# Optimization experiments

Hardware: AMD Instinct MI355X
Metric: run time of the kernel (lower is better)

The kernel has to match this reference:

```python
import jax, jax.numpy as jnp
import numpy as np

N_NODES = 100000


def _add_self_loops(edge_index, n):
    loop = jnp.arange(n, dtype=edge_index.dtype)
    src = jnp.concatenate([edge_index[0], loop])
    dst = jnp.concatenate([edge_index[1], loop])
    return src, dst


def _gcn_conv(x, W, b, src, dst, n):
    # PyG GCNConv: add_self_loops + symmetric normalization + linear + scatter-add
    deg = jax.ops.segment_sum(jnp.ones_like(dst, dtype=x.dtype), dst, num_segments=n)
    dinv = jnp.where(deg > 0, jax.lax.rsqrt(deg), 0.0)
    h = x @ W  # [N, F_out]
    norm = dinv[src] * dinv[dst]            # [E]
    msg = h[src] * norm[:, None]            # gather + scale, [E, F_out]
    out = jax.ops.segment_sum(msg, dst, num_segments=n)
    return out + b


def setup_inputs() -> dict:
    key = jax.random.key(0)
    k1, k2, k3, k4 = jax.random.split(key, 4)
    d = 128
    E = 1600000
    x = jax.random.normal(k1, (N_NODES, d), dtype=jnp.float32)
    edge_index = jax.random.randint(k2, (2, E), 0, N_NODES, dtype=jnp.int64)
    # Glorot-ish scaling for the linear weights
    s = 1.0 / np.sqrt(d)
    W1 = jax.random.normal(k3, (d, d), dtype=jnp.float32) * s
    W2 = jax.random.normal(k4, (d, d), dtype=jnp.float32) * s
    b1 = jnp.zeros((d,), dtype=jnp.float32)
    b2 = jnp.zeros((d,), dtype=jnp.float32)
    return {"x": x, "edge_index": edge_index, "W1": W1, "b1": b1, "W2": W2, "b2": b2}


def reference(x, edge_index, W1, b1, W2, b2):
    n = x.shape[0]
    src, dst = _add_self_loops(edge_index, n)
    h = jax.nn.relu(_gcn_conv(x, W1, b1, src, dst, n))
    out = _gcn_conv(h, W2, b2, src, dst, n)
    # original does x.view(1600) (= N * out_channels for its 40x40 toy size);
    # generalized: flatten to [N * out_channels]
    return out.reshape(-1)
```

## Files before the change

kernel.cpp:

```cpp
#include <hip/hip_runtime.h>

static inline int idiv_up(int a, int b) { return (a + b - 1) / b; }

typedef __attribute__((ext_vector_type(8))) short bf16x8;
typedef __attribute__((ext_vector_type(4))) float f32x4;

#define NBSHIFT 10
#define BCAP    20480
#define EPB     4096

__device__ __forceinline__ float bf16u_to_f32(unsigned short u) {
    return __uint_as_float(((unsigned int)u) << 16);
}

__device__ __forceinline__ unsigned short f32_to_bf16u(float x) {
    unsigned int b = __float_as_uint(x);
    b += 0x7FFFu + ((b >> 16) & 1u);
    return (unsigned short)(b >> 16);
}

__global__ void k_binit(int* __restrict__ bucketCur) {
    if (threadIdx.x < 128) bucketCur[threadIdx.x] = threadIdx.x * BCAP;
}

__global__ __launch_bounds__(256) void k_bucketA(const int* __restrict__ src,
                                                 const int* __restrict__ dst, int E,
                                                 int* __restrict__ bucketCur,
                                                 int* __restrict__ tmp) {
    __shared__ int bh[128];
    __shared__ int bbase[128];
    const int c0 = blockIdx.x * EPB;
    const int cend = min(c0 + EPB, E);
    const int tid = threadIdx.x;
    if (tid < 128) bh[tid] = 0;
    __syncthreads();
    for (int i = c0 + tid; i < cend; i += 256)
        atomicAdd(&bh[dst[i] >> NBSHIFT], 1);
    __syncthreads();
    if (tid < 128) {
        const int c = bh[tid];
        bbase[tid] = c ? atomicAdd(&bucketCur[tid], c) : 0;
        bh[tid] = 0;
    }
    __syncthreads();
    for (int i = c0 + tid; i < cend; i += 256) {
        const int d = dst[i];
        const int b = d >> NBSHIFT;
        const int loc = atomicAdd(&bh[b], 1);
        tmp[bbase[b] + loc] = ((d & ((1 << NBSHIFT) - 1)) << 17) | src[i];
    }
}

__global__ __launch_bounds__(1024) void k_build(const int* __restrict__ tmp,
                                                const int* __restrict__ bucketCur,
                                                int* __restrict__ rowptr,
                                                int* __restrict__ cnt,
                                                float* __restrict__ dinv,
                                                int* __restrict__ csr, int N) {
    __shared__ int h[1024];
    __shared__ int sc[1024];
    const int b = blockIdx.x;
    const int tid = threadIdx.x;
    const int beg = b * BCAP;
    const int ecnt = bucketCur[b] - beg;
    const int node0 = b << NBSHIFT;

    h[tid] = 0;
    __syncthreads();
    for (int i = tid; i < ecnt; i += 1024)
        atomicAdd(&h[tmp[beg + i] >> 17], 1);
    __syncthreads();

    const int v = h[tid];
    sc[tid] = v;
    __syncthreads();
#pragma unroll
    for (int off = 1; off < 1024; off <<= 1) {
        int x = 0;
        if (tid >= off) x = sc[tid - off];
        __syncthreads();
        if (tid >= off) sc[tid] += x;
        __syncthreads();
    }
    const int rowbase = beg + sc[tid] - v;
    const int node = node0 + tid;
    if (node < N) {
        rowptr[node] = rowbase;
        cnt[node]    = v;
        dinv[node]   = rsqrtf((float)v + 1.0f);
    }
    __syncthreads();
    h[tid] = rowbase;
    __syncthreads();
    for (int i = tid; i < ecnt; i += 1024) {
        const int p = tmp[beg + i];
        const int pos = atomicAdd(&h[p >> 17], 1);
        csr[pos] = p & 0x1FFFF;
    }
}

template<bool ABF16>
__global__ __launch_bounds__(256) void k_gemm(const void* __restrict__ Av,
                                              const float* __restrict__ W,
                                              const float* __restrict__ dinv,
                                              unsigned short* __restrict__ C, int N) {
    __shared__ unsigned short Wt[128 * 128];
    const int tid = threadIdx.x;

    {
        const int col = tid >> 1;
        const int k0  = (tid & 1) * 64;
#pragma unroll
        for (int i = 0; i < 8; ++i) {
            bf16x8 pk;
#pragma unroll
            for (int j = 0; j < 8; ++j)
                pk[j] = (short)f32_to_bf16u(W[(size_t)(k0 + i * 8 + j) * 128 + col]);
            const int kus = k0 + i * 8;
            *(bf16x8*)&Wt[col * 128 + (kus ^ ((col & 7) << 3))] = pk;
        }
    }
    __syncthreads();

    const int wave = tid >> 6;
    const int lane = tid & 63;
    const int lrow = lane & 15;
    const int lgrp = lane >> 4;
    const int rbase = blockIdx.x * 128 + wave * 32;

    f32x4 acc[2][8];
#pragma unroll
    for (int r = 0; r < 2; ++r)
#pragma unroll
        for (int c = 0; c < 8; ++c) acc[r][c] = (f32x4){0.f, 0.f, 0.f, 0.f};

#pragma unroll
    for (int kk = 0; kk < 4; ++kk) {
        const int kbase = kk * 32 + lgrp * 8;
        bf16x8 afrag[2];
#pragma unroll
        for (int r = 0; r < 2; ++r) {
            const int row = rbase + r * 16 + lrow;
            bf16x8 a = (bf16x8){0, 0, 0, 0, 0, 0, 0, 0};
            if (row < N) {
                if constexpr (ABF16) {
                    a = *(const bf16x8*)((const unsigned short*)Av + (size_t)row * 128 + kbase);
                } else {
                    const float* p = (const float*)Av + (size_t)row * 128 + kbase;
                    const float4 f0 = *(const float4*)p;
                    const float4 f1 = *(const float4*)(p + 4);
                    a[0] = (short)f32_to_bf16u(f0.x); a[1] = (short)f32_to_bf16u(f0.y);
                    a[2] = (short)f32_to_bf16u(f0.z); a[3] = (short)f32_to_bf16u(f0.w);
                    a[4] = (short)f32_to_bf16u(f1.x); a[5] = (short)f32_to_bf16u(f1.y);
                    a[6] = (short)f32_to_bf16u(f1.z); a[7] = (short)f32_to_bf16u(f1.w);
                }
            }
            afrag[r] = a;
        }
#pragma unroll
        for (int c = 0; c < 8; ++c) {
            const int col = c * 16 + lrow;
            const bf16x8 bb = *(const bf16x8*)&Wt[col * 128 + (kbase ^ ((col & 7) << 3))];
            acc[0][c] = __builtin_amdgcn_mfma_f32_16x16x32_bf16(afrag[0], bb, acc[0][c], 0, 0, 0);
            acc[1][c] = __builtin_amdgcn_mfma_f32_16x16x32_bf16(afrag[1], bb, acc[1][c], 0, 0, 0);
        }
    }

#pragma unroll
    for (int r = 0; r < 2; ++r) {
#pragma unroll
        for (int reg = 0; reg < 4; ++reg) {
            const int orow = rbase + r * 16 + lgrp * 4 + reg;
            if (orow < N) {
                const float dv = dinv[orow];
                unsigned short* crow = C + (size_t)orow * 128 + lrow;
#pragma unroll
                for (int c = 0; c < 8; ++c)
                    crow[c * 16] = f32_to_bf16u(acc[r][c][reg] * dv);
            }
        }
    }
}

template<int OUT_BF16_RELU>
__global__ __launch_bounds__(256) void k_pull(const int* __restrict__ rowptr,
                                              const int* __restrict__ cnt,
                                              const int* __restrict__ csr,
                                              const unsigned short* __restrict__ t,
                                              const float* __restrict__ dinv,
                                              const float* __restrict__ bias,
                                              void* __restrict__ outv, int N) {
    const int nid = blockIdx.x * 4 + (threadIdx.x >> 6);
    if (nid >= N) return;
    const int lane2 = (threadIdx.x & 63) * 2;
    const int beg = rowptr[nid];
    const int end = beg + cnt[nid];

    float acc0 = 0.f, acc1 = 0.f;
    int j = beg;

    for (; j + 16 <= end; j += 16) {
        int s[16];
#pragma unroll
        for (int q = 0; q < 16; ++q) s[q] = csr[j + q];
        ushort2 u[16];
#pragma unroll
        for (int q = 0; q < 16; ++q)
            u[q] = *(const ushort2*)(t + (size_t)s[q] * 128 + lane2);
#pragma unroll
        for (int q = 0; q < 16; ++q) {
            acc0 += bf16u_to_f32(u[q].x);
            acc1 += bf16u_to_f32(u[q].y);
        }
    }
    if (j + 8 <= end) {
        int s[8];
#pragma unroll
        for (int q = 0; q < 8; ++q) s[q] = csr[j + q];
        ushort2 u[8];
#pragma unroll
        for (int q = 0; q < 8; ++q)
            u[q] = *(const ushort2*)(t + (size_t)s[q] * 128 + lane2);
#pragma unroll
        for (int q = 0; q < 8; ++q) {
            acc0 += bf16u_to_f32(u[q].x);
            acc1 += bf16u_to_f32(u[q].y);
        }
        j += 8;
    }
    if (j + 4 <= end) {
        int s[4];
#pragma unroll
        for (int q = 0; q < 4; ++q) s[q] = csr[j + q];
        ushort2 u[4];
#pragma unroll
        for (int q = 0; q < 4; ++q)
            u[q] = *(const ushort2*)(t + (size_t)s[q] * 128 + lane2);
#pragma unroll
        for (int q = 0; q < 4; ++q) {
            acc0 += bf16u_to_f32(u[q].x);
            acc1 += bf16u_to_f32(u[q].y);
        }
        j += 4;
    }
    for (; j + 2 <= end; j += 2) {
        const int s0 = csr[j];
        const int s1 = csr[j + 1];
        const ushort2 u0 = *(const ushort2*)(t + (size_t)s0 * 128 + lane2);
        const ushort2 u1 = *(const ushort2*)(t + (size_t)s1 * 128 + lane2);
        acc0 += bf16u_to_f32(u0.x); acc1 += bf16u_to_f32(u0.y);
        acc0 += bf16u_to_f32(u1.x); acc1 += bf16u_to_f32(u1.y);
    }
    if (j < end) {
        const ushort2 u = *(const ushort2*)(t + (size_t)csr[j] * 128 + lane2);
        acc0 += bf16u_to_f32(u.x); acc1 += bf16u_to_f32(u.y);
    }

    const float dd = dinv[nid];
    const ushort2 us = *(const ushort2*)(t + (size_t)nid * 128 + lane2);
    const float2 b = *(const float2*)(bias + lane2);
    acc0 = (acc0 + bf16u_to_f32(us.x)) * dd + b.x;
    acc1 = (acc1 + bf16u_to_f32(us.y)) * dd + b.y;
    if (OUT_BF16_RELU) {
        acc0 = fmaxf(acc0, 0.f); acc1 = fmaxf(acc1, 0.f);
        ushort2 o; o.x = f32_to_bf16u(acc0); o.y = f32_to_bf16u(acc1);
        *(ushort2*)((unsigned short*)outv + (size_t)nid * 128 + lane2) = o;
    } else {
        *(float2*)((float*)outv + (size_t)nid * 128 + lane2) = make_float2(acc0, acc1);
    }
}

extern "C" void kernel_launch(void* const* d_in, const int* in_sizes, int n_in,
                              void* d_out, int out_size, void* d_ws, size_t ws_size,
                              hipStream_t stream) {
    const float* x   = (const float*)d_in[0];
    const int*   ei  = (const int*)d_in[1];
    const float* W1  = (const float*)d_in[2];
    const float* b1  = (const float*)d_in[3];
    const float* W2  = (const float*)d_in[4];
    const float* b2  = (const float*)d_in[5];
    float*       out = (float*)d_out;

    const int N = in_sizes[0] / 128;
    const int E = in_sizes[1] / 2;
    const int* esrc = ei;
    const int* edst = ei + E;
    const size_t NF = (size_t)N * 128;
    const int nbk = idiv_up(N, 1 << NBSHIFT);
    const int ebl = idiv_up(E, EPB);

    char* ws = (char*)d_ws;
    size_t o = 0;
    int*   bucketCur = (int*)(ws + o);   o += 128 * 4;              o = (o + 255) & ~(size_t)255;
    int*   rowptr    = (int*)(ws + o);   o += (size_t)N * 4;        o = (o + 255) & ~(size_t)255;
    int*   cnt       = (int*)(ws + o);   o += (size_t)N * 4;        o = (o + 255) & ~(size_t)255;
    float* dinv      = (float*)(ws + o); o += (size_t)N * 4;        o = (o + 255) & ~(size_t)255;
    unsigned short* t = (unsigned short*)(ws + o); o += NF * 2;     o = (o + 255) & ~(size_t)255;
    unsigned short* h = (unsigned short*)(ws + o); o += NF * 2;     o = (o + 255) & ~(size_t)255;
    int*   tmp       = (int*)(ws + o);   o += (size_t)(nbk + 1) * BCAP * 4; o = (o + 255) & ~(size_t)255;
    int*   csr       = (int*)(ws + o);   o += (size_t)(nbk + 1) * BCAP * 4;

    k_binit  <<<1, 128, 0, stream>>>(bucketCur);
    k_bucketA<<<ebl, 256, 0, stream>>>(esrc, edst, E, bucketCur, tmp);
    k_build  <<<nbk, 1024, 0, stream>>>(tmp, bucketCur, rowptr, cnt, dinv, csr, N);

    const int gblocks = idiv_up(N, 128);
    const int pblocks = idiv_up(N, 4);

    k_gemm<false><<<gblocks, 256, 0, stream>>>(x, W1, dinv, t, N);
    k_pull<1>    <<<pblocks, 256, 0, stream>>>(rowptr, cnt, csr, t, dinv, b1, h, N);

    k_gemm<true> <<<gblocks, 256, 0, stream>>>(h, W2, dinv, t, N);
    k_pull<0>    <<<pblocks, 256, 0, stream>>>(rowptr, cnt, csr, t, dinv, b2, out, N);
}
```

Before: 222.6 us.

## Use finer CSR buckets, vectorized edge loads, wave-shuffle scan, packed rowptr/count

```diff
diff --git a/kernel.cpp b/kernel.cpp
--- a/kernel.cpp
+++ b/kernel.cpp
@@ -5,8 +5,8 @@
 typedef __attribute__((ext_vector_type(8))) short bf16x8;
 typedef __attribute__((ext_vector_type(4))) float f32x4;
 
-#define NBSHIFT 10
-#define BCAP    20480
+#define NBSHIFT 9
+#define BCAP    11264
 #define EPB     4096
 
 __device__ __forceinline__ float bf16u_to_f32(unsigned short u) {
@@ -20,45 +20,65 @@
 }
 
 __global__ void k_binit(int* __restrict__ bucketCur) {
-    if (threadIdx.x < 128) bucketCur[threadIdx.x] = threadIdx.x * BCAP;
+    if (threadIdx.x < 256) bucketCur[threadIdx.x] = threadIdx.x * BCAP;
 }
 
 __global__ __launch_bounds__(256) void k_bucketA(const int* __restrict__ src,
                                                  const int* __restrict__ dst, int E,
                                                  int* __restrict__ bucketCur,
                                                  int* __restrict__ tmp) {
-    __shared__ int bh[128];
-    __shared__ int bbase[128];
+    __shared__ int bh[256];
+    __shared__ int bbase[256];
+    const int tid = threadIdx.x;
     const int c0 = blockIdx.x * EPB;
     const int cend = min(c0 + EPB, E);
-    const int tid = threadIdx.x;
-    if (tid < 128) bh[tid] = 0;
-    __syncthreads();
-    for (int i = c0 + tid; i < cend; i += 256)
-        atomicAdd(&bh[dst[i] >> NBSHIFT], 1);
-    __syncthreads();
-    if (tid < 128) {
+    bh[tid] = 0;
+    __syncthreads();
+
+    int sv[16], dv[16];
+#pragma unroll
+    for (int i = 0; i < 4; ++i) {
+        const int p = c0 + i * 1024 + tid * 4;
+        int4 s4 = make_int4(0, 0, 0, 0);
+        int4 d4 = make_int4(-1, -1, -1, -1);
+        if (p + 4 <= cend) {
+            s4 = *(const int4*)(src + p);
+            d4 = *(const int4*)(dst + p);
+        } else if (p < cend) {
+            s4.x = src[p]; d4.x = dst[p];
+            if (p + 1 < cend) { s4.y = src[p + 1]; d4.y = dst[p + 1]; }
+            if (p + 2 < cend) { s4.z = src[p + 2]; d4.z = dst[p + 2]; }
+        }
+        sv[i * 4 + 0] = s4.x; sv[i * 4 + 1] = s4.y; sv[i * 4 + 2] = s4.z; sv[i * 4 + 3] = s4.w;
+        dv[i * 4 + 0] = d4.x; dv[i * 4 + 1] = d4.y; dv[i * 4 + 2] = d4.z; dv[i * 4 + 3] = d4.w;
+    }
+#pragma unroll
+    for (int i = 0; i < 16; ++i)
+        if (dv[i] >= 0) atomicAdd(&bh[dv[i] >> NBSHIFT], 1);
+    __syncthreads();
+    {
         const int c = bh[tid];
         bbase[tid] = c ? atomicAdd(&bucketCur[tid], c) : 0;
         bh[tid] = 0;
     }
     __syncthreads();
-    for (int i = c0 + tid; i < cend; i += 256) {
-        const int d = dst[i];
-        const int b = d >> NBSHIFT;
-        const int loc = atomicAdd(&bh[b], 1);
-        tmp[bbase[b] + loc] = ((d & ((1 << NBSHIFT) - 1)) << 17) | src[i];
-    }
-}
-
-__global__ __launch_bounds__(1024) void k_build(const int* __restrict__ tmp,
-                                                const int* __restrict__ bucketCur,
-                                                int* __restrict__ rowptr,
-                                                int* __restrict__ cnt,
-                                                float* __restrict__ dinv,
-                                                int* __restrict__ csr, int N) {
-    __shared__ int h[1024];
-    __shared__ int sc[1024];
+#pragma unroll
+    for (int i = 0; i < 16; ++i) {
+        if (dv[i] >= 0) {
+            const int b = dv[i] >> NBSHIFT;
+            const int loc = atomicAdd(&bh[b], 1);
+            tmp[bbase[b] + loc] = ((dv[i] & ((1 << NBSHIFT) - 1)) << 17) | sv[i];
+        }
+    }
+}
+
+__global__ __launch_bounds__(512) void k_build(const int* __restrict__ tmp,
+                                               const int* __restrict__ bucketCur,
+                                               int2* __restrict__ rowcnt,
+                                               float* __restrict__ dinv,
+                                               int* __restrict__ csr, int N) {
+    __shared__ int h[512];
+    __shared__ int woff[9];
     const int b = blockIdx.x;
     const int tid = threadIdx.x;
     const int beg = b * BCAP;
@@ -67,32 +87,37 @@
 
     h[tid] = 0;
     __syncthreads();
-    for (int i = tid; i < ecnt; i += 1024)
+    for (int i = tid; i < ecnt; i += 512)
         atomicAdd(&h[tmp[beg + i] >> 17], 1);
     __syncthreads();
 
     const int v = h[tid];
-    sc[tid] = v;
-    __syncthreads();
-#pragma unroll
-    for (int off = 1; off < 1024; off <<= 1) {
-        int x = 0;
-        if (tid >= off) x = sc[tid - off];
-        __syncthreads();
-        if (tid >= off) sc[tid] += x;
-        __syncthreads();
-    }
-    const int rowbase = beg + sc[tid] - v;
+    const int lane = tid & 63;
+    const int w = tid >> 6;
+    int incl = v;
+#pragma unroll
+    for (int off = 1; off < 64; off <<= 1) {
+        const int y = __shfl_up(incl, off, 64);
+        if (lane >= off) incl += y;
+    }
+    if (lane == 63) woff[w + 1] = incl;
+    if (tid == 0) woff[0] = 0;
+    __syncthreads();
+    if (tid == 0) {
+#pragma unroll
+        for (int i = 1; i < 8; ++i) woff[i + 1] += woff[i];
+    }
+    __syncthreads();
+    const int rowbase = beg + woff[w] + incl - v;
     const int node = node0 + tid;
     if (node < N) {
-        rowptr[node] = rowbase;
-        cnt[node]    = v;
+        rowcnt[node] = make_int2(rowbase, v);
         dinv[node]   = rsqrtf((float)v + 1.0f);
     }
     __syncthreads();
     h[tid] = rowbase;
     __syncthreads();
-    for (int i = tid; i < ecnt; i += 1024) {
+    for (int i = tid; i < ecnt; i += 512) {
         const int p = tmp[beg + i];
         const int pos = atomicAdd(&h[p >> 17], 1);
         csr[pos] = p & 0x1FFFF;
@@ -183,8 +208,7 @@
 }
 
 template<int OUT_BF16_RELU>
-__global__ __launch_bounds__(256) void k_pull(const int* __restrict__ rowptr,
-                                              const int* __restrict__ cnt,
+__global__ __launch_bounds__(256) void k_pull(const int2* __restrict__ rowcnt,
                                               const int* __restrict__ csr,
                                               const unsigned short* __restrict__ t,
                                               const float* __restrict__ dinv,
@@ -193,8 +217,13 @@
     const int nid = blockIdx.x * 4 + (threadIdx.x >> 6);
     if (nid >= N) return;
     const int lane2 = (threadIdx.x & 63) * 2;
-    const int beg = rowptr[nid];
-    const int end = beg + cnt[nid];
+    const int2 rc = rowcnt[nid];
+    const int beg = rc.x;
+    const int end = rc.x + rc.y;
+
+    const float dd = dinv[nid];
+    const ushort2 us = *(const ushort2*)(t + (size_t)nid * 128 + lane2);
+    const float2 bvec = *(const float2*)(bias + lane2);
 
     float acc0 = 0.f, acc1 = 0.f;
     int j = beg;
@@ -256,11 +285,8 @@
         acc0 += bf16u_to_f32(u.x); acc1 += bf16u_to_f32(u.y);
     }
 
-    const float dd = dinv[nid];
-    const ushort2 us = *(const ushort2*)(t + (size_t)nid * 128 + lane2);
-    const float2 b = *(const float2*)(bias + lane2);
-    acc0 = (acc0 + bf16u_to_f32(us.x)) * dd + b.x;
-    acc1 = (acc1 + bf16u_to_f32(us.y)) * dd + b.y;
+    acc0 = (acc0 + bf16u_to_f32(us.x)) * dd + bvec.x;
+    acc1 = (acc1 + bf16u_to_f32(us.y)) * dd + bvec.y;
     if (OUT_BF16_RELU) {
         acc0 = fmaxf(acc0, 0.f); acc1 = fmaxf(acc1, 0.f);
         ushort2 o; o.x = f32_to_bf16u(acc0); o.y = f32_to_bf16u(acc1);
@@ -291,25 +317,24 @@
 
     char* ws = (char*)d_ws;
     size_t o = 0;
-    int*   bucketCur = (int*)(ws + o);   o += 128 * 4;              o = (o + 255) & ~(size_t)255;
-    int*   rowptr    = (int*)(ws + o);   o += (size_t)N * 4;        o = (o + 255) & ~(size_t)255;
-    int*   cnt       = (int*)(ws + o);   o += (size_t)N * 4;        o = (o + 255) & ~(size_t)255;
+    int*   bucketCur = (int*)(ws + o);   o += 256 * 4;              o = (o + 255) & ~(size_t)255;
+    int2*  rowcnt    = (int2*)(ws + o);  o += (size_t)N * 8;        o = (o + 255) & ~(size_t)255;
     float* dinv      = (float*)(ws + o); o += (size_t)N * 4;        o = (o + 255) & ~(size_t)255;
     unsigned short* t = (unsigned short*)(ws + o); o += NF * 2;     o = (o + 255) & ~(size_t)255;
     unsigned short* h = (unsigned short*)(ws + o); o += NF * 2;     o = (o + 255) & ~(size_t)255;
     int*   tmp       = (int*)(ws + o);   o += (size_t)(nbk + 1) * BCAP * 4; o = (o + 255) & ~(size_t)255;
     int*   csr       = (int*)(ws + o);   o += (size_t)(nbk + 1) * BCAP * 4;
 
-    k_binit  <<<1, 128, 0, stream>>>(bucketCur);
+    k_binit  <<<1, 256, 0, stream>>>(bucketCur);
     k_bucketA<<<ebl, 256, 0, stream>>>(esrc, edst, E, bucketCur, tmp);
-    k_build  <<<nbk, 1024, 0, stream>>>(tmp, bucketCur, rowptr, cnt, dinv, csr, N);
+    k_build  <<<nbk, 512, 0, stream>>>(tmp, bucketCur, rowcnt, dinv, csr, N);
 
     const int gblocks = idiv_up(N, 128);
     const int pblocks = idiv_up(N, 4);
 
     k_gemm<false><<<gblocks, 256, 0, stream>>>(x, W1, dinv, t, N);
-    k_pull<1>    <<<pblocks, 256, 0, stream>>>(rowptr, cnt, csr, t, dinv, b1, h, N);
+    k_pull<1>    <<<pblocks, 256, 0, stream>>>(rowcnt, csr, t, dinv, b1, h, N);
 
     k_gemm<true> <<<gblocks, 256, 0, stream>>>(h, W2, dinv, t, N);
-    k_pull<0>    <<<pblocks, 256, 0, stream>>>(rowptr, cnt, csr, t, dinv, b2, out, N);
-}
+    k_pull<0>    <<<pblocks, 256, 0, stream>>>(rowcnt, csr, t, dinv, b2, out, N);
+}
```

Measured after the change: 209.9 us (median of 2 runs). 1.06x faster.
